# Kernel optimization log

Measured on AMD Instinct MI355X. Metric: run time of the kernel, lower is better.

The kernel has to match this reference:

```python
import jax, jax.numpy as jnp
import numpy as np

# Static network layout: inputs occupy columns [0, I), hidden [I, N-O), outputs [N-O, N)
B = 16384  # batch size
N = 1024   # total neurons
I = 128    # input neurons
O = 64     # output neurons
REFRACTORY = 0.9


def _activate(x, act_ids):
    """Vectorized per-neuron heterogeneous activation.
    act_ids: 0=relu, 1=tanh, 2=sigmoid, 3=identity.
    Replaces the original serial per-neuron getattr dispatch loop."""
    r = jax.nn.relu(x)
    t = jnp.tanh(x)
    s = jax.nn.sigmoid(x)
    return jnp.select([act_ids == 0, act_ids == 1, act_ids == 2], [r, t, s], x)


def setup_inputs() -> dict:
    key = jax.random.key(0)
    k0, k1, k2, k3, k4 = jax.random.split(key, 5)
    return {
        "prev_states": jax.random.normal(k0, (B, N), jnp.float32),
        "input_values": jax.random.normal(k1, (B, I), jnp.float32),
        "weight_matrix": jax.random.normal(k2, (N, N), jnp.float32) * 0.05,
        "biases": jax.random.normal(k3, (N,), jnp.float32) * 0.1,
        "act_ids": jax.random.randint(k4, (N,), 0, 4, dtype=jnp.int32),
    }


def reference(prev_states, input_values, weight_matrix, biases, act_ids):
    # _apply_refractory_factor on hidden cols + _assign_input_values on input cols
    states = jnp.concatenate(
        [input_values,
         prev_states[:, I:N - O] * REFRACTORY,
         prev_states[:, N - O:]],
        axis=1)  # [B, N]
    # total_input = states @ W + b
    total = states @ weight_matrix + biases  # [B, N]
    # activation applied to every non-input neuron; input neurons keep their state
    activated = _activate(total, act_ids[None, :])  # [B, N]
    new_states = jnp.concatenate([states[:, :I], activated[:, I:]], axis=1)
    # return output-layer slice
    return new_states[:, N - O:]
```

## Files before the change

kernel.cpp:

```cpp
#include <hip/hip_runtime.h>
#include <math.h>

#define BATCH 16384
#define NN    1024
#define NI    128
#define NO    64
#define REFR  0.9f

typedef float  f32x4  __attribute__((ext_vector_type(4)));
typedef __bf16 bf16x8 __attribute__((ext_vector_type(8)));

__global__ __launch_bounds__(256) void pack_w_kernel(const float* __restrict__ W,
                                                     __bf16* __restrict__ wsB) {
    int idx = blockIdx.x * 256 + threadIdx.x;
    int j  = idx & 7;
    int l  = (idx >> 3) & 63;
    int tn = (idx >> 9) & 3;
    int kc = idx >> 11;
    int k  = kc * 32 + (l >> 4) * 8 + j;
    int n  = tn * 16 + (l & 15);
    wsB[idx] = (__bf16)W[(size_t)k * NN + (NN - NO) + n];
}

__device__ inline float activate(float x, int id) {
    if (id == 0) return fmaxf(x, 0.0f);
    if (id == 1) return tanhf(x);
    if (id == 2) return 1.0f / (1.0f + __expf(-x));
    return x;
}

__global__ __launch_bounds__(256) void fused_rnn_kernel(
    const float* __restrict__ prev,
    const float* __restrict__ inp,
    const __bf16* __restrict__ wsB,
    const float* __restrict__ bias,
    const int*  __restrict__ act,
    float* __restrict__ out)
{
    const int lane = threadIdx.x & 63;
    const int wv   = threadIdx.x >> 6;
    const int m    = lane & 15;
    const int q    = lane >> 4;
    const int row0 = blockIdx.x * 64 + wv * 16;
    const int rowA = row0 + m;

    const float* prow = prev + (size_t)rowA * NN;
    const float* irow = inp  + (size_t)rowA * NI;
    const bf16x8* Bf  = (const bf16x8*)wsB;

    f32x4 acc[4];
    acc[0] = (f32x4){0.f, 0.f, 0.f, 0.f};
    acc[1] = acc[0]; acc[2] = acc[0]; acc[3] = acc[0];

    const int qo = q * 8;

#define K_STEP(kc, srcRow, scale)                                              \
    {                                                                          \
        const float4* p = (const float4*)((srcRow) + (kc) * 32 + qo);          \
        float4 f0 = p[0];                                                      \
        float4 f1 = p[1];                                                      \
        bf16x8 a;                                                              \
        a[0] = (__bf16)(f0.x * (scale)); a[1] = (__bf16)(f0.y * (scale));      \
        a[2] = (__bf16)(f0.z * (scale)); a[3] = (__bf16)(f0.w * (scale));      \
        a[4] = (__bf16)(f1.x * (scale)); a[5] = (__bf16)(f1.y * (scale));      \
        a[6] = (__bf16)(f1.z * (scale)); a[7] = (__bf16)(f1.w * (scale));      \
        const bf16x8* bp = Bf + (size_t)(kc) * 256 + lane;                     \
        acc[0] = __builtin_amdgcn_mfma_f32_16x16x32_bf16(a, bp[0],   acc[0], 0, 0, 0); \
        acc[1] = __builtin_amdgcn_mfma_f32_16x16x32_bf16(a, bp[64],  acc[1], 0, 0, 0); \
        acc[2] = __builtin_amdgcn_mfma_f32_16x16x32_bf16(a, bp[128], acc[2], 0, 0, 0); \
        acc[3] = __builtin_amdgcn_mfma_f32_16x16x32_bf16(a, bp[192], acc[3], 0, 0, 0); \
    }

#pragma unroll
    for (int kc = 0; kc < 4; ++kc) K_STEP(kc, irow, 1.0f)

#pragma unroll 4
    for (int kc = 4; kc < 30; ++kc) K_STEP(kc, prow, REFR)

#pragma unroll
    for (int kc = 30; kc < 32; ++kc) K_STEP(kc, prow, 1.0f)

#undef K_STEP

    const float* bo = bias + (NN - NO);
    const int*   ao = act  + (NN - NO);
#pragma unroll
    for (int t = 0; t < 4; ++t) {
        const int col = t * 16 + m;
        const float bb = bo[col];
        const int   id = ao[col];
#pragma unroll
        for (int r = 0; r < 4; ++r) {
            const int rr = row0 + q * 4 + r;
            out[(size_t)rr * NO + col] = activate(acc[t][r] + bb, id);
        }
    }
}

extern "C" void kernel_launch(void* const* d_in, const int* in_sizes, int n_in,
                              void* d_out, int out_size, void* d_ws, size_t ws_size,
                              hipStream_t stream) {
    const float* prev = (const float*)d_in[0];
    const float* inp  = (const float*)d_in[1];
    const float* W    = (const float*)d_in[2];
    const float* bias = (const float*)d_in[3];
    const int*   act  = (const int*)  d_in[4];
    float* out = (float*)d_out;
    __bf16* wsB = (__bf16*)d_ws;

    pack_w_kernel<<<256, 256, 0, stream>>>(W, wsB);

    fused_rnn_kernel<<<BATCH / 64, 256, 0, stream>>>(prev, inp, wsB, bias, act, out);
}
```

Baseline: 121.7 us.

## Split K across waves with LDS reduction, one 16-row tile per block

Each block now handles 16 rows instead of 64, and its four waves each take one quarter of the K dimension (8 chunks of 32) instead of all 32 chunks. Partial accumulators are reduced through shared memory, then bias and activation are applied and the result is written as vectorized float4 stores. The aim is a 4x larger grid (1024 blocks) with shorter per-wave dependency chains, so the memory-bound read of prev_states has more parallelism in flight. The cost is an LDS round trip and a block barrier, and launch_bounds now asks for four blocks per CU.

```diff
diff --git a/kernel.cpp b/kernel.cpp
--- a/kernel.cpp
+++ b/kernel.cpp
@@ -29,7 +29,7 @@
     return x;
 }
 
-__global__ __launch_bounds__(256) void fused_rnn_kernel(
+__global__ __launch_bounds__(256, 4) void fused_rnn_kernel(
     const float* __restrict__ prev,
     const float* __restrict__ inp,
     const __bf16* __restrict__ wsB,
@@ -41,7 +41,8 @@
     const int wv   = threadIdx.x >> 6;
     const int m    = lane & 15;
     const int q    = lane >> 4;
-    const int row0 = blockIdx.x * 64 + wv * 16;
+    const int tile = blockIdx.x;
+    const int row0 = tile * 16;
     const int rowA = row0 + m;
 
     const float* prow = prev + (size_t)rowA * NN;
@@ -54,47 +55,58 @@
 
     const int qo = q * 8;
 
-#define K_STEP(kc, srcRow, scale)                                              \
-    {                                                                          \
-        const float4* p = (const float4*)((srcRow) + (kc) * 32 + qo);          \
-        float4 f0 = p[0];                                                      \
-        float4 f1 = p[1];                                                      \
-        bf16x8 a;                                                              \
-        a[0] = (__bf16)(f0.x * (scale)); a[1] = (__bf16)(f0.y * (scale));      \
-        a[2] = (__bf16)(f0.z * (scale)); a[3] = (__bf16)(f0.w * (scale));      \
-        a[4] = (__bf16)(f1.x * (scale)); a[5] = (__bf16)(f1.y * (scale));      \
-        a[6] = (__bf16)(f1.z * (scale)); a[7] = (__bf16)(f1.w * (scale));      \
-        const bf16x8* bp = Bf + (size_t)(kc) * 256 + lane;                     \
-        acc[0] = __builtin_amdgcn_mfma_f32_16x16x32_bf16(a, bp[0],   acc[0], 0, 0, 0); \
-        acc[1] = __builtin_amdgcn_mfma_f32_16x16x32_bf16(a, bp[64],  acc[1], 0, 0, 0); \
-        acc[2] = __builtin_amdgcn_mfma_f32_16x16x32_bf16(a, bp[128], acc[2], 0, 0, 0); \
-        acc[3] = __builtin_amdgcn_mfma_f32_16x16x32_bf16(a, bp[192], acc[3], 0, 0, 0); \
+#pragma unroll
+    for (int i = 0; i < 8; ++i) {
+        const int kc = wv * 8 + i;
+        const float* srcRow = (kc < 4) ? irow : prow;
+        const float  scale  = (kc >= 4 && kc < 30) ? REFR : 1.0f;
+
+        const float4* p = (const float4*)(srcRow + kc * 32 + qo);
+        float4 f0 = p[0];
+        float4 f1 = p[1];
+        bf16x8 a;
+        a[0] = (__bf16)(f0.x * scale); a[1] = (__bf16)(f0.y * scale);
+        a[2] = (__bf16)(f0.z * scale); a[3] = (__bf16)(f0.w * scale);
+        a[4] = (__bf16)(f1.x * scale); a[5] = (__bf16)(f1.y * scale);
+        a[6] = (__bf16)(f1.z * scale); a[7] = (__bf16)(f1.w * scale);
+
+        const bf16x8* bp = Bf + (size_t)kc * 256 + lane;
+        acc[0] = __builtin_amdgcn_mfma_f32_16x16x32_bf16(a, bp[0],   acc[0], 0, 0, 0);
+        acc[1] = __builtin_amdgcn_mfma_f32_16x16x32_bf16(a, bp[64],  acc[1], 0, 0, 0);
+        acc[2] = __builtin_amdgcn_mfma_f32_16x16x32_bf16(a, bp[128], acc[2], 0, 0, 0);
+        acc[3] = __builtin_amdgcn_mfma_f32_16x16x32_bf16(a, bp[192], acc[3], 0, 0, 0);
     }
 
+    __shared__ float red[4][16][68];
 #pragma unroll
-    for (int kc = 0; kc < 4; ++kc) K_STEP(kc, irow, 1.0f)
+    for (int t = 0; t < 4; ++t) {
+#pragma unroll
+        for (int r = 0; r < 4; ++r) {
+            red[wv][q * 4 + r][t * 16 + m] = acc[t][r];
+        }
+    }
+    __syncthreads();
 
-#pragma unroll 4
-    for (int kc = 4; kc < 30; ++kc) K_STEP(kc, prow, REFR)
+    const int orow = threadIdx.x >> 4;
+    const int oc   = (threadIdx.x & 15) * 4;
 
-#pragma unroll
-    for (int kc = 30; kc < 32; ++kc) K_STEP(kc, prow, 1.0f)
-
-#undef K_STEP
+    f32x4 s;
+    {
+        const f32x4* p0 = (const f32x4*)&red[0][orow][oc];
+        const f32x4* p1 = (const f32x4*)&red[1][orow][oc];
+        const f32x4* p2 = (const f32x4*)&red[2][orow][oc];
+        const f32x4* p3 = (const f32x4*)&red[3][orow][oc];
+        s = *p0 + *p1 + *p2 + *p3;
+    }
 
     const float* bo = bias + (NN - NO);
     const int*   ao = act  + (NN - NO);
+    f32x4 o;
 #pragma unroll
-    for (int t = 0; t < 4; ++t) {
-        const int col = t * 16 + m;
-        const float bb = bo[col];
-        const int   id = ao[col];
-#pragma unroll
-        for (int r = 0; r < 4; ++r) {
-            const int rr = row0 + q * 4 + r;
-            out[(size_t)rr * NO + col] = activate(acc[t][r] + bb, id);
-        }
+    for (int c = 0; c < 4; ++c) {
+        o[c] = activate(s[c] + bo[oc + c], ao[oc + c]);
     }
+    *(f32x4*)(out + (size_t)(row0 + orow) * NO + oc) = o;
 }
 
 extern "C" void kernel_launch(void* const* d_in, const int* in_sizes, int n_in,
@@ -110,5 +122,5 @@
 
     pack_w_kernel<<<256, 256, 0, stream>>>(W, wsB);
 
-    fused_rnn_kernel<<<BATCH / 64, 256, 0, stream>>>(prev, inp, wsB, bias, act, out);
+    fused_rnn_kernel<<<BATCH / 16, 256, 0, stream>>>(prev, inp, wsB, bias, act, out);
 }
```

Measured after the change: 117.7 us. 3.4% less time.
